# Kernel optimization log

Hardware: AMD Instinct MI355X
Metric: run time of the kernel (lower is better)

## Reference

```python
import jax, jax.numpy as jnp
import numpy as np

NC = 1      # constants.nc (Game-of-Life grid channels)
GRID = 32
PAD_ITERS = 31


def _iterated_wrap_idx(n, p):
    # Faithfully simulate p iterations of circular pad-1 on a growing axis.
    # NOTE: this is NOT a single wrap-pad of p; the border alternates 0/n-1.
    idx = np.arange(n)
    for _ in range(p):
        idx = np.concatenate([idx[-1:], idx, idx[:1]])
    return jnp.asarray(idx)

_IDX = _iterated_wrap_idx(GRID, PAD_ITERS)  # length 94, static


def _pad(x):
    # one gather per spatial dim replaces the 31-iteration concat loop
    return x[:, :, _IDX][:, :, :, _IDX]


def _conv(x, w, b, stride):
    y = jax.lax.conv_general_dilated(
        x, w, window_strides=(stride, stride), padding='VALID',
        dimension_numbers=('NCHW', 'OIHW', 'NCHW'))
    return y + b[None, :, None, None]


def setup_inputs() -> dict:
    key = jax.random.key(0)
    ks = jax.random.split(key, 7)
    B = 16
    s_in = 1.0 / np.sqrt(NC * 32 * 32)      # fan-in init, keeps activations sane
    s_hid = 1.0 / np.sqrt(32 * 32 * 32)
    s_out = 1.0 / np.sqrt(32)
    return {
        'x': jax.random.normal(ks[0], (B, NC, GRID, GRID), jnp.float32),
        'in_w': jax.random.normal(ks[1], (32, NC, 32, 32), jnp.float32) * s_in,
        'in_b': jnp.zeros((32,), jnp.float32),
        'convs_w': jax.random.normal(ks[2], (20, 32, 32, 32, 32), jnp.float32) * s_hid,
        'convs_b': jnp.zeros((20, 32), jnp.float32),
        'out_w': jax.random.normal(ks[3], (NC, 32, 1, 1), jnp.float32) * s_out,
        'out_b': jnp.zeros((NC,), jnp.float32),
    }


def reference(x, in_w, in_b, convs_w, convs_b, out_w, out_b):
    # in_conv: pad(31 iters) + conv k=32 s=2 (no ReLU, as in original)
    h = _conv(_pad(x), in_w, in_b, 2)           # [B,32,32,32]

    def step(h, wb):
        w, b = wb
        h = jax.nn.relu(_conv(_pad(h), w, b, 2))
        return h, None

    h, _ = jax.lax.scan(step, h, (convs_w, convs_b))  # 20 hidden layers
    return _conv(h, out_w, out_b, 1)             # 1x1 out conv, no activation
```

## Files before the change

### kernel.cpp

```cpp
#include <hip/hip_runtime.h>


typedef _Float16 f16;
typedef _Float16 f16x8 __attribute__((ext_vector_type(8)));
typedef float f32x4 __attribute__((ext_vector_type(4)));
typedef float f32x16 __attribute__((ext_vector_type(16)));

__device__ __forceinline__ int mwrap(int j) {
  int t = j - 31;
  if ((unsigned)t <= 31u) return t;
  if (t < 0) return (j & 1) ? 0 : 31;
  return (j & 1) ? 0 : 31;
}


#define LOADF(FD, cc)                                                       \
  {                                                                         \
    const int so_ = ((cc) & 7) * 6144;                                      \
    _Pragma("unroll")                                                       \
    for (int j_ = 0; j_ < 6; ++j_) {                                        \
      const int* Rj_ = (const int*)(lds0 + V[j_] + so_);                    \
      int4 t0_, t1_;                                                        \
      t0_.x = Rj_[0]; t0_.y = Rj_[1]; t0_.z = Rj_[2]; t0_.w = Rj_[3];       \
      t1_.x = Rj_[8]; t1_.y = Rj_[9]; t1_.z = Rj_[10]; t1_.w = Rj_[11];     \
      FD[j_][0] = __builtin_bit_cast(f16x8, t0_);                           \
      FD[j_][1] = __builtin_bit_cast(f16x8, t1_);                           \
    }                                                                       \
  }

#define MFMAC(AUSE, FD)                                                     \
  {                                                                         \
    _Pragma("unroll")                                                       \
    for (int kyi_ = 0; kyi_ < 4; ++kyi_) {                                  \
      _Pragma("unroll")                                                     \
      for (int kxh_ = 0; kxh_ < 2; ++kxh_) {                                \
        const f16x8 a_ = AUSE[kyi_ * 2 + kxh_];                             \
        acc0 = __builtin_amdgcn_mfma_f32_32x32x16_f16(a_, FD[kyi_][kxh_],   \
                                                      acc0, 0, 0, 0);       \
        acc1 = __builtin_amdgcn_mfma_f32_32x32x16_f16(a_, FD[kyi_ + 2][kxh_],\
                                                      acc1, 0, 0, 0);       \
      }                                                                     \
    }                                                                       \
  }

#define GOLBAR()                                       \
  asm volatile("s_waitcnt lgkmcnt(0)" ::: "memory");   \
  __builtin_amdgcn_sched_barrier(0);                   \
  __builtin_amdgcn_s_barrier();

template <int CIN, bool RELU, bool PRE>
__global__ __launch_bounds__(512, 2) void gemm3(
    const void* __restrict__ Wv,
    const f16* __restrict__ hp_in,
    const float* __restrict__ bias,
    f16* __restrict__ hp_out) {
  __shared__ __align__(16) f16 rowbuf[8][32][96];
  __shared__ float Red[8][2][1024];

  const int tid = threadIdx.x;
  const int lane = tid & 63;
  const int w = tid >> 6;
  const int ox = lane & 31;
  const int s = lane >> 5;

  const int pair0 = blockIdx.x * 2;
  const int b = pair0 >> 5;
  const int oy0 = pair0 & 31;

  const int rrow = tid / 12, rseg = tid - rrow * 12;

  const int bi = ox + 4 * s;
  char* lds0 = (char*)&rowbuf[0][0][0];
  int V[6];
#pragma unroll
  for (int j = 0; j < 6; ++j)
    V[j] = mwrap(2 * oy0 + 4 * w + j) * 192 + bi * 4;

  const int wroff = rrow * 192 + rseg * 16;

  f32x16 acc0 = {}, acc1 = {};
  f16x8 A0[8], A1[8];
  f16x8 F0[6][2], F1[6][2];
  f16x8 stgA = {}, stgB = {}, stgC = {}, stgD = {};

  auto loadA = [&](int c, f16x8* dst) {
#pragma unroll
    for (int kyi = 0; kyi < 4; ++kyi) {
#pragma unroll
      for (int kxh = 0; kxh < 2; ++kxh) {
        const int ky = 4 * w + kyi;
        const int chunk = (c * 32 + ky) * 2 + kxh;
        if constexpr (PRE) {
          const f16* Wl = (const f16*)Wv;
          dst[kyi * 2 + kxh] = *(const f16x8*)(Wl + (size_t)chunk * 512 + lane * 8);
        } else {
          const float* Wl = (const float*)Wv;
          const float* sp = Wl + (((size_t)(ox * CIN + c) * 32 + ky) * 32 + kxh * 16 + s * 8);
          f32x4 u0 = *(const f32x4*)sp;
          f32x4 u1 = *(const f32x4*)(sp + 4);
          f16x8 v;
          v[0] = (f16)u0[0]; v[1] = (f16)u0[1]; v[2] = (f16)u0[2]; v[3] = (f16)u0[3];
          v[4] = (f16)u1[0]; v[5] = (f16)u1[1]; v[6] = (f16)u1[2]; v[7] = (f16)u1[3];
          dst[kyi * 2 + kxh] = v;
        }
      }
    }
  };
  auto loadRowTo = [&](int c, f16x8& dst) {
    if (tid < 384)
      dst = *(const f16x8*)(hp_in + ((size_t)(b * CIN + c) * 32 + rrow) * 96 + rseg * 8);
  };
  auto writeSlot = [&](int slot, const f16x8& src) {
    if (tid < 384) *(f16x8*)(lds0 + slot * 6144 + wroff) = src;
  };

  if constexpr (CIN == 1) {
    loadRowTo(0, stgA);
    writeSlot(0, stgA);
    loadA(0, A0);
    __syncthreads();
    LOADF(F0, 0);
    MFMAC(A0, F0);
  } else {
    static_assert(CIN % 4 == 0, "CIN must be 1 or a multiple of 4");
    loadRowTo(0, stgA); loadRowTo(1, stgB);
    loadRowTo(2, stgC); loadRowTo(3, stgD);
    writeSlot(0, stgA); writeSlot(1, stgB);
    writeSlot(2, stgC); writeSlot(3, stgD);
    loadA(0, A0);
    __syncthreads();

#pragma unroll 1
    for (int g = 0; g < CIN / 4; ++g) {
      const int t0 = 4 * g;
      const bool more = (t0 + 4 < CIN);
      if (more) {
        loadRowTo(t0 + 4, stgA); loadRowTo(t0 + 5, stgB);
        loadRowTo(t0 + 6, stgC); loadRowTo(t0 + 7, stgD);
      }
      LOADF(F0, t0);
      loadA(t0 + 1, A1);
      LOADF(F1, t0 + 1);
      MFMAC(A0, F0);
      LOADF(F0, t0 + 2);
      loadA(t0 + 2, A0);
      MFMAC(A1, F1);
      LOADF(F1, t0 + 3);
      loadA(t0 + 3, A1);
      MFMAC(A0, F0);
      if (more) {
        writeSlot((t0 + 4) & 7, stgA); writeSlot((t0 + 5) & 7, stgB);
        writeSlot((t0 + 6) & 7, stgC); writeSlot((t0 + 7) & 7, stgD);
        loadA(t0 + 4, A0);
      }
      MFMAC(A1, F1);
      GOLBAR();
    }
  }

#pragma unroll
  for (int r = 0; r < 16; ++r) {
    Red[w][0][r * 64 + lane] = acc0[r];
    Red[w][1][r * 64 + lane] = acc1[r];
  }
  __syncthreads();

#pragma unroll
  for (int k4 = 0; k4 < 4; ++k4) {
    const int o = tid + 512 * k4;
    const int p = o >> 10, co = (o >> 5) & 31, oxx = o & 31;
    const int idx = ((co & 3) + 4 * (co >> 3)) * 64 + ((co >> 2) & 1) * 32 + oxx;
    float v = bias[co];
#pragma unroll
    for (int w8 = 0; w8 < 8; ++w8) v += Red[w8][p][idx];
    if (RELU) v = fmaxf(v, 0.f);
    const f16 hv = (f16)v;
    f16* base = hp_out + ((size_t)(b * 32 + co) * 32 + (oy0 + p)) * 96;
    base[oxx + 31] = hv;
    if (oxx == 0) {
#pragma unroll
      for (int j = 1; j <= 29; j += 2) base[j] = hv;
#pragma unroll
      for (int j = 63; j <= 93; j += 2) base[j] = hv;
    }
    if (oxx == 31) {
#pragma unroll
      for (int j = 0; j <= 30; j += 2) base[j] = hv;
#pragma unroll
      for (int j = 64; j <= 92; j += 2) base[j] = hv;
    }
  }
}

__global__ void pad_x_kernel(const float* __restrict__ x, f16* __restrict__ xp) {
  const int i = blockIdx.x * 256 + threadIdx.x;
  if (i >= 48128) return;
  const int bq = i / 3008, r = i - bq * 3008;
  const int y = r / 94, j = r - y * 94;
  xp[bq * 3072 + y * 96 + j] = (f16)x[(bq * 32 + y) * 32 + mwrap(j)];
}

__global__ void convert_w3(const float* __restrict__ in_w,
                           const float* __restrict__ convs_w,
                           f16* __restrict__ WfIn, f16* __restrict__ WfH) {
  const int total = 4096 + 20 * 131072;
  for (int g = blockIdx.x * blockDim.x + threadIdx.x; g < total;
       g += gridDim.x * blockDim.x) {
    const float* src;
    f16* dst;
    int chunk, lanE, c, ky, kxh;
    if (g < 4096) {
      chunk = g >> 6; lanE = g & 63;
      kxh = chunk & 1; ky = chunk >> 1; c = 0;
      const int co = lanE & 31, ss = lanE >> 5;
      src = in_w + ((size_t)(co * 1 + 0) * 32 + ky) * 32 + kxh * 16 + ss * 8;
      dst = WfIn + (size_t)chunk * 512 + lanE * 8;
    } else {
      const int h = g - 4096;
      const int layer = h >> 17, r = h & 131071;
      chunk = r >> 6; lanE = r & 63;
      kxh = chunk & 1;
      const int t = chunk >> 1;
      ky = t & 31; c = t >> 5;
      const int co = lanE & 31, ss = lanE >> 5;
      src = convs_w + (size_t)layer * 1048576 +
            ((size_t)(co * 32 + c) * 32 + ky) * 32 + kxh * 16 + ss * 8;
      dst = WfH + (size_t)layer * 1048576 + (size_t)chunk * 512 + lanE * 8;
    }
    f32x4 u0 = *(const f32x4*)src;
    f32x4 u1 = *(const f32x4*)(src + 4);
    f16x8 v;
    v[0] = (f16)u0[0]; v[1] = (f16)u0[1]; v[2] = (f16)u0[2]; v[3] = (f16)u0[3];
    v[4] = (f16)u1[0]; v[5] = (f16)u1[1]; v[6] = (f16)u1[2]; v[7] = (f16)u1[3];
    *(f16x8*)dst = v;
  }
}

__global__ void out_conv3(const f16* __restrict__ hp,
                          const float* __restrict__ ow,
                          const float* __restrict__ ob,
                          float* __restrict__ out) {
  const int o = blockIdx.x * 256 + threadIdx.x;
  const int b = o >> 10, oy = (o >> 5) & 31, oxx = o & 31;
  float s = ob[0];
#pragma unroll
  for (int c = 0; c < 32; ++c)
    s += ow[c] * (float)hp[((size_t)(b * 32 + c) * 32 + oy) * 96 + oxx + 31];
  out[o] = s;
}

extern "C" void kernel_launch(void* const* d_in, const int* in_sizes, int n_in,
                              void* d_out, int out_size, void* d_ws,
                              size_t ws_size, hipStream_t stream) {
  const float* x = (const float*)d_in[0];
  const float* in_w = (const float*)d_in[1];
  const float* in_b = (const float*)d_in[2];
  const float* convs_w = (const float*)d_in[3];
  const float* convs_b = (const float*)d_in[4];
  const float* out_w = (const float*)d_in[5];
  const float* out_b = (const float*)d_in[6];
  float* out = (float*)d_out;

  char* ws = (char*)d_ws;
  f16* xpad = (f16*)ws;
  f16* hpA = (f16*)(ws + 98304);
  f16* hpB = (f16*)(ws + 98304 + 3145728);
  f16* WfIn = (f16*)(ws + 6389760);
  f16* WfH = (f16*)(ws + 6455296);
  const bool pre = (ws_size >= 48398336ull);

  pad_x_kernel<<<188, 256, 0, stream>>>(x, xpad);
  if (pre) convert_w3<<<2048, 256, 0, stream>>>(in_w, convs_w, WfIn, WfH);

  if (pre)
    gemm3<1, false, true><<<256, 512, 0, stream>>>(WfIn, xpad, in_b, hpA);
  else
    gemm3<1, false, false><<<256, 512, 0, stream>>>(in_w, xpad, in_b, hpA);

  for (int l = 0; l < 20; ++l) {
    const f16* cur = (l % 2 == 0) ? hpA : hpB;
    f16* nxt = (l % 2 == 0) ? hpB : hpA;
    if (pre)
      gemm3<32, true, true><<<256, 512, 0, stream>>>(
          WfH + (size_t)l * 1048576, cur, convs_b + 32 * l, nxt);
    else
      gemm3<32, true, false><<<256, 512, 0, stream>>>(
          convs_w + (size_t)l * 1048576, cur, convs_b + 32 * l, nxt);
  }

  out_conv3<<<64, 256, 0, stream>>>(hpA, out_w, out_b, out);
}
```

Before: 987.7 us.

## Split each block to one output row, shrink LDS and double occupancy

Each block now computes a single output row instead of two, halving per-block accumulators, fragment registers and the LDS ring (4 slots, reduction buffer aliased onto row buffer), and launches twice as many blocks with launch bounds raised to 4 blocks per CU. Block indices are swizzled so neighbouring blocks map to different batch/row groups. The deeper software pipeline (A double-buffering and 4-channel staging) is replaced by a simpler 2-channel loop. The aim is more waves per CU to hide latency, at the cost of reloading each weight fragment for every row, which doubles weight traffic, and less intra-wave overlap.

```diff
diff --git a/kernel.cpp b/kernel.cpp
--- a/kernel.cpp
+++ b/kernel.cpp
@@ -16,9 +16,9 @@
 
 #define LOADF(FD, cc)                                                       \
   {                                                                         \
-    const int so_ = ((cc) & 7) * 6144;                                      \
+    const int so_ = ((cc) & 3) * 6144;                                      \
     _Pragma("unroll")                                                       \
-    for (int j_ = 0; j_ < 6; ++j_) {                                        \
+    for (int j_ = 0; j_ < 4; ++j_) {                                        \
       const int* Rj_ = (const int*)(lds0 + V[j_] + so_);                    \
       int4 t0_, t1_;                                                        \
       t0_.x = Rj_[0]; t0_.y = Rj_[1]; t0_.z = Rj_[2]; t0_.w = Rj_[3];       \
@@ -34,11 +34,8 @@
     for (int kyi_ = 0; kyi_ < 4; ++kyi_) {                                  \
       _Pragma("unroll")                                                     \
       for (int kxh_ = 0; kxh_ < 2; ++kxh_) {                                \
-        const f16x8 a_ = AUSE[kyi_ * 2 + kxh_];                             \
-        acc0 = __builtin_amdgcn_mfma_f32_32x32x16_f16(a_, FD[kyi_][kxh_],   \
-                                                      acc0, 0, 0, 0);       \
-        acc1 = __builtin_amdgcn_mfma_f32_32x32x16_f16(a_, FD[kyi_ + 2][kxh_],\
-                                                      acc1, 0, 0, 0);       \
+        acc0 = __builtin_amdgcn_mfma_f32_32x32x16_f16(                      \
+            AUSE[kyi_ * 2 + kxh_], FD[kyi_][kxh_], acc0, 0, 0, 0);          \
       }                                                                     \
     }                                                                       \
   }
@@ -49,13 +46,14 @@
   __builtin_amdgcn_s_barrier();
 
 template <int CIN, bool RELU, bool PRE>
-__global__ __launch_bounds__(512, 2) void gemm3(
+__global__ __launch_bounds__(512, 4) void gemm3(
     const void* __restrict__ Wv,
     const f16* __restrict__ hp_in,
     const float* __restrict__ bias,
     f16* __restrict__ hp_out) {
-  __shared__ __align__(16) f16 rowbuf[8][32][96];
-  __shared__ float Red[8][2][1024];
+  __shared__ __align__(16) char smem[32768];
+  char* lds0 = smem;
+  float* Red = (float*)smem;
 
   const int tid = threadIdx.x;
   const int lane = tid & 63;
@@ -63,25 +61,25 @@
   const int ox = lane & 31;
   const int s = lane >> 5;
 
-  const int pair0 = blockIdx.x * 2;
+  const int bid = blockIdx.x;
+  const int pair0 = ((bid & 7) << 6) | (bid >> 3);
   const int b = pair0 >> 5;
-  const int oy0 = pair0 & 31;
+  const int oy = pair0 & 31;
 
   const int rrow = tid / 12, rseg = tid - rrow * 12;
 
   const int bi = ox + 4 * s;
-  char* lds0 = (char*)&rowbuf[0][0][0];
-  int V[6];
-#pragma unroll
-  for (int j = 0; j < 6; ++j)
-    V[j] = mwrap(2 * oy0 + 4 * w + j) * 192 + bi * 4;
+  int V[4];
+#pragma unroll
+  for (int j = 0; j < 4; ++j)
+    V[j] = mwrap(2 * oy + 4 * w + j) * 192 + bi * 4;
 
   const int wroff = rrow * 192 + rseg * 16;
 
-  f32x16 acc0 = {}, acc1 = {};
-  f16x8 A0[8], A1[8];
-  f16x8 F0[6][2], F1[6][2];
-  f16x8 stgA = {}, stgB = {}, stgC = {}, stgD = {};
+  f32x16 acc0 = {};
+  f16x8 A[8];
+  f16x8 F[4][2];
+  f16x8 stgA = {}, stgB = {};
 
   auto loadA = [&](int c, f16x8* dst) {
 #pragma unroll
@@ -117,65 +115,54 @@
   if constexpr (CIN == 1) {
     loadRowTo(0, stgA);
     writeSlot(0, stgA);
-    loadA(0, A0);
+    loadA(0, A);
     __syncthreads();
-    LOADF(F0, 0);
-    MFMAC(A0, F0);
+    LOADF(F, 0);
+    MFMAC(A, F);
   } else {
-    static_assert(CIN % 4 == 0, "CIN must be 1 or a multiple of 4");
+    static_assert(CIN % 2 == 0, "CIN must be 1 or even");
     loadRowTo(0, stgA); loadRowTo(1, stgB);
-    loadRowTo(2, stgC); loadRowTo(3, stgD);
     writeSlot(0, stgA); writeSlot(1, stgB);
-    writeSlot(2, stgC); writeSlot(3, stgD);
-    loadA(0, A0);
     __syncthreads();
 
 #pragma unroll 1
-    for (int g = 0; g < CIN / 4; ++g) {
-      const int t0 = 4 * g;
-      const bool more = (t0 + 4 < CIN);
+    for (int c0 = 0; c0 < CIN; c0 += 2) {
+      const bool more = (c0 + 2 < CIN);
       if (more) {
-        loadRowTo(t0 + 4, stgA); loadRowTo(t0 + 5, stgB);
-        loadRowTo(t0 + 6, stgC); loadRowTo(t0 + 7, stgD);
+        loadRowTo(c0 + 2, stgA);
+        loadRowTo(c0 + 3, stgB);
       }
-      LOADF(F0, t0);
-      loadA(t0 + 1, A1);
-      LOADF(F1, t0 + 1);
-      MFMAC(A0, F0);
-      LOADF(F0, t0 + 2);
-      loadA(t0 + 2, A0);
-      MFMAC(A1, F1);
-      LOADF(F1, t0 + 3);
-      loadA(t0 + 3, A1);
-      MFMAC(A0, F0);
+      loadA(c0, A);
+      LOADF(F, c0);
+      MFMAC(A, F);
+      loadA(c0 + 1, A);
+      LOADF(F, c0 + 1);
+      MFMAC(A, F);
       if (more) {
-        writeSlot((t0 + 4) & 7, stgA); writeSlot((t0 + 5) & 7, stgB);
-        writeSlot((t0 + 6) & 7, stgC); writeSlot((t0 + 7) & 7, stgD);
-        loadA(t0 + 4, A0);
+        writeSlot((c0 + 2) & 3, stgA);
+        writeSlot((c0 + 3) & 3, stgB);
       }
-      MFMAC(A1, F1);
       GOLBAR();
     }
   }
 
-#pragma unroll
-  for (int r = 0; r < 16; ++r) {
-    Red[w][0][r * 64 + lane] = acc0[r];
-    Red[w][1][r * 64 + lane] = acc1[r];
-  }
   __syncthreads();
 
 #pragma unroll
-  for (int k4 = 0; k4 < 4; ++k4) {
-    const int o = tid + 512 * k4;
-    const int p = o >> 10, co = (o >> 5) & 31, oxx = o & 31;
+  for (int r = 0; r < 16; ++r) Red[w * 1024 + r * 64 + lane] = acc0[r];
+  __syncthreads();
+
+#pragma unroll
+  for (int k2 = 0; k2 < 2; ++k2) {
+    const int o = tid + 512 * k2;
+    const int co = (o >> 5) & 31, oxx = o & 31;
     const int idx = ((co & 3) + 4 * (co >> 3)) * 64 + ((co >> 2) & 1) * 32 + oxx;
     float v = bias[co];
 #pragma unroll
-    for (int w8 = 0; w8 < 8; ++w8) v += Red[w8][p][idx];
+    for (int w8 = 0; w8 < 8; ++w8) v += Red[w8 * 1024 + idx];
     if (RELU) v = fmaxf(v, 0.f);
     const f16 hv = (f16)v;
-    f16* base = hp_out + ((size_t)(b * 32 + co) * 32 + (oy0 + p)) * 96;
+    f16* base = hp_out + ((size_t)(b * 32 + co) * 32 + oy) * 96;
     base[oxx + 31] = hv;
     if (oxx == 0) {
 #pragma unroll
@@ -273,18 +260,18 @@
   if (pre) convert_w3<<<2048, 256, 0, stream>>>(in_w, convs_w, WfIn, WfH);
 
   if (pre)
-    gemm3<1, false, true><<<256, 512, 0, stream>>>(WfIn, xpad, in_b, hpA);
+    gemm3<1, false, true><<<512, 512, 0, stream>>>(WfIn, xpad, in_b, hpA);
   else
-    gemm3<1, false, false><<<256, 512, 0, stream>>>(in_w, xpad, in_b, hpA);
+    gemm3<1, false, false><<<512, 512, 0, stream>>>(in_w, xpad, in_b, hpA);
 
   for (int l = 0; l < 20; ++l) {
     const f16* cur = (l % 2 == 0) ? hpA : hpB;
     f16* nxt = (l % 2 == 0) ? hpB : hpA;
     if (pre)
-      gemm3<32, true, true><<<256, 512, 0, stream>>>(
+      gemm3<32, true, true><<<512, 512, 0, stream>>>(
           WfH + (size_t)l * 1048576, cur, convs_b + 32 * l, nxt);
     else
-      gemm3<32, true, false><<<256, 512, 0, stream>>>(
+      gemm3<32, true, false><<<512, 512, 0, stream>>>(
           convs_w + (size_t)l * 1048576, cur, convs_b + 32 * l, nxt);
   }
 
```

Measured after the change: 1.175 ms. +18.9%, slower.
